# Optimization experiments

Measured on AMD Instinct MI355X. Metric: run time of the kernel, lower is better.

## Reference

```python
import jax, jax.numpy as jnp
import numpy as np

A = 32          # num input capsule types
PSIZE = 16      # caps_size (pose matrix 4x4)
MD = 4          # mat_dim = sqrt(caps_size)
NCLS = 10       # output capsules / classes
KF = 5          # routing kernel (final_shape)
KK = KF * KF
KKA = KK * A
ITERS = 3
FINAL_LAMBDA = 0.01
EPS = 1e-12
LN2PI = float(np.log(2.0 * np.pi))
BN_EPS = 1e-5


def unfold(x, k, stride, pad):
    # torch.nn.functional.unfold: [b,C,h,w] -> [b, C*k*k, L], (c, kh, kw) channel-major
    b, c, h, w = x.shape
    if pad:
        x = jnp.pad(x, ((0, 0), (0, 0), (pad, pad), (pad, pad)))
    oh = (h + 2 * pad - k) // stride + 1
    ow = (w + 2 * pad - k) // stride + 1
    cols = jnp.stack([
        jnp.stack([x[:, :, i:i + stride * oh:stride, j:j + stride * ow:stride]
                   for j in range(k)], axis=3)
        for i in range(k)], axis=2)          # [b, c, k, k, oh, ow]
    return cols.reshape(b, c * k * k, oh * ow)


def conv3x3(x, w):
    return jax.lax.conv_general_dilated(x, w, (1, 1), [(1, 1), (1, 1)],
                                        dimension_numbers=('NCHW', 'OIHW', 'NCHW'))


def bn_inf(x, g, b, m, v):
    scale = g / jnp.sqrt(v + BN_EPS)
    return (x - m[None, :, None, None]) * scale[None, :, None, None] + b[None, :, None, None]


def em_routing(a_in, pose, W, beta_u, beta_a):
    b = a_in.shape[0]
    # pose votes
    pu = unfold(pose, KF, 1, 0)                     # [b, A*PSIZE*KK, l]
    l = pu.shape[-1]
    pu = pu.reshape(b, A, PSIZE, KK, l).transpose(0, 4, 3, 1, 2).reshape(b, l, KKA, PSIZE)
    pm = pu.reshape(b, l, KKA, MD, MD)[:, :, :, None]        # [b,l,kkA,1,md,md]
    v = jnp.matmul(pm, W)                                    # [b,l,kkA,B,md,md]
    v = v.reshape(b, l, KKA, NCLS, PSIZE)
    # activations
    au = unfold(a_in, KF, 1, 0).reshape(b, A, KK, l).transpose(0, 3, 2, 1).reshape(b, l, KKA)
    r = jnp.ones((b, l, KKA, NCLS, 1), v.dtype)
    a_out = mu = None
    for i in range(ITERS):
        lam = FINAL_LAMBDA * (1.0 - 0.95 ** (i + 1))
        # M-step
        rw = r * au[:, :, :, None, None]
        r_sum = rw.sum(axis=2, keepdims=True)                # [b,l,1,B,1]
        coeff = rw / (r_sum + EPS)
        mu = (coeff * v).sum(axis=2, keepdims=True)          # [b,l,1,B,psize]
        sigma_sq = (coeff * (v - mu) ** 2).sum(axis=2, keepdims=True) + EPS
        r_s = r_sum[:, :, 0]                                 # [b,l,B,1]
        sig = sigma_sq[:, :, 0]                              # [b,l,B,psize]
        cost_h = (beta_u + 0.5 * jnp.log(sig)) * r_s         # log(sqrt(s)) = 0.5*log(s)
        a_out = jax.nn.sigmoid(lam * (beta_a - cost_h.sum(axis=3)))   # [b,l,B]
        if i < ITERS - 1:
            # E-step (note: log(sigma_sq * ln2pi) as in original code)
            ln_p = (-0.5 * jnp.sum(jnp.log(sigma_sq * LN2PI), axis=-1)
                    - jnp.sum((v - mu) ** 2 / (2.0 * sigma_sq), axis=-1))   # [b,l,kkA,B]
            ln_ap = ln_p + jnp.log(a_out)[:, :, None, :]
            r = jax.nn.softmax(ln_ap, axis=-1)[..., None]
    oh = int(np.floor(np.sqrt(l)))
    pose_out = mu[:, :, 0].reshape(b, l, -1).transpose(0, 2, 1).reshape(b, -1, oh, oh)
    a_map = a_out.transpose(0, 2, 1).reshape(b, -1, oh, oh)
    return a_map, pose_out


def setup_inputs():
    key = jax.random.key(0)
    ks = jax.random.split(key, 14)
    batch = 256
    x = jax.random.normal(ks[0], (batch, 512, 5, 5), jnp.float32)
    w_a = jax.random.normal(ks[1], (A, 512, 3, 3), jnp.float32) * 0.02
    w_pose = jax.random.normal(ks[2], (A * PSIZE, 512, 3, 3), jnp.float32) * 0.02
    bn_a_g = 1.0 + 0.1 * jax.random.normal(ks[3], (A,), jnp.float32)
    bn_a_b = 0.1 * jax.random.normal(ks[4], (A,), jnp.float32)
    bn_a_m = 0.1 * jax.random.normal(ks[5], (A,), jnp.float32)
    bn_a_v = jax.random.uniform(ks[6], (A,), jnp.float32, 0.5, 1.5)
    C2 = A * PSIZE
    bn_p_g = 1.0 + 0.1 * jax.random.normal(ks[7], (C2,), jnp.float32)
    bn_p_b = 0.1 * jax.random.normal(ks[8], (C2,), jnp.float32)
    bn_p_m = 0.1 * jax.random.normal(ks[9], (C2,), jnp.float32)
    bn_p_v = jax.random.uniform(ks[10], (C2,), jnp.float32, 0.5, 1.5)
    W = jax.random.normal(ks[11], (KKA, NCLS, MD, MD), jnp.float32) * 0.25
    beta_u = jnp.zeros((1, 1, NCLS, 1), jnp.float32)
    beta_a = jnp.zeros((1, 1, NCLS), jnp.float32)
    return {"x": x, "w_a": w_a, "w_pose": w_pose,
            "bn_a_g": bn_a_g, "bn_a_b": bn_a_b, "bn_a_m": bn_a_m, "bn_a_v": bn_a_v,
            "bn_p_g": bn_p_g, "bn_p_b": bn_p_b, "bn_p_m": bn_p_m, "bn_p_v": bn_p_v,
            "W": W, "beta_u": beta_u, "beta_a": beta_a}


def reference(x, w_a, w_pose, bn_a_g, bn_a_b, bn_a_m, bn_a_v,
              bn_p_g, bn_p_b, bn_p_m, bn_p_v, W, beta_u, beta_a):
    a = jax.nn.sigmoid(bn_inf(conv3x3(x, w_a), bn_a_g, bn_a_b, bn_a_m, bn_a_v))
    pose = bn_inf(conv3x3(x, w_pose), bn_p_g, bn_p_b, bn_p_m, bn_p_v)
    a_map, _ = em_routing(a, pose, W, beta_u, beta_a)
    out = a_map.reshape(a_map.shape[0], -1)          # [b, 10]
    out = out / out.sum(axis=1, keepdims=True)
    return jnp.log(out)
```

## Files before the change

kernel.cpp:

```cpp
#include <hip/hip_runtime.h>
#include <math.h>

#define CIN 512
#define NCLS 10
#define KDIM 4608
#define NTOT 6400
#define MPAD 640
#define BK 128
#define NKT 36
#define NABLK (5 * NKT)
#define LN2PI_F 1.8378770664093453f

typedef __attribute__((ext_vector_type(8))) short bf16x8;
typedef __attribute__((ext_vector_type(4))) float f32x4;

typedef const __attribute__((address_space(1))) void* gas_ptr;
typedef __attribute__((address_space(3))) void* las_ptr;

__device__ __forceinline__ void async_copy16(const void* g, void* l) {
    __builtin_amdgcn_global_load_lds((gas_ptr)g, (las_ptr)l, 16, 0, 0);
}

__device__ __forceinline__ unsigned short f2bf(float f) {
    unsigned int u = __float_as_uint(f);
    u = (u + 0x7fffu + ((u >> 16) & 1u)) >> 16;
    return (unsigned short)u;
}
__device__ __forceinline__ float fexp(float x) { return __expf(x); }
__device__ __forceinline__ float flog(float x) { return __logf(x); }

__global__ __launch_bounds__(256) void pack_a_kernel(
    const float* __restrict__ w_pose, const float* __restrict__ w_a,
    const float* __restrict__ bn_p_g, const float* __restrict__ bn_p_b,
    const float* __restrict__ bn_p_m, const float* __restrict__ bn_p_v,
    const float* __restrict__ bn_a_g, const float* __restrict__ bn_a_b,
    const float* __restrict__ bn_a_m, const float* __restrict__ bn_a_v,
    const float* __restrict__ Wm,
    unsigned short* __restrict__ At, unsigned short* __restrict__ Wmb,
    float* __restrict__ sc, float* __restrict__ bi)
{
    const int blk = blockIdx.x;
    const int t = threadIdx.x;

    if (blk >= NABLK) {
        const int chunk = (blk - NABLK) * 256 + t;
        if (chunk < 16000) {
            const float4* s4 = reinterpret_cast<const float4*>(Wm + (size_t)chunk * 8);
            float4 x0 = s4[0], x1 = s4[1];
            int4 o;
            o.x = (int)f2bf(x0.x) | ((int)f2bf(x0.y) << 16);
            o.y = (int)f2bf(x0.z) | ((int)f2bf(x0.w) << 16);
            o.z = (int)f2bf(x1.x) | ((int)f2bf(x1.y) << 16);
            o.w = (int)f2bf(x1.z) | ((int)f2bf(x1.w) << 16);
            reinterpret_cast<int4*>(Wmb + (size_t)chunk * 8)[0] = o;
        }
        return;
    }

    const int mblk = blk / NKT;
    if (blk == 0) {
        for (int i = t; i < MPAD; i += 256) {
            float s = 0.f, b = 0.f;
            if (i < 512) {
                s = bn_p_g[i] / sqrtf(bn_p_v[i] + 1e-5f);
                b = bn_p_b[i] - bn_p_m[i] * s;
            } else if (i < 544) {
                const int j = i - 512;
                s = bn_a_g[j] / sqrtf(bn_a_v[j] + 1e-5f);
                b = bn_a_b[j] - bn_a_m[j] * s;
            }
            sc[i] = s; bi[i] = b;
        }
    }

    const int kt = blk - mblk * NKT;
    #pragma unroll
    for (int j = 0; j < 8; ++j) {
        const int c = t + j * 256;
        const int kc8 = c >> 7, slot = c & 127;
        const int row = mblk * 128 + (slot ^ (kc8 << 2));
        const int k0 = (kt * 16 + kc8) * 8;
        float v[8] = {0.f,0.f,0.f,0.f,0.f,0.f,0.f,0.f};
        if (row < 512) {
            const float4* s4 = reinterpret_cast<const float4*>(w_pose + (size_t)row * KDIM + k0);
            float4 x0 = s4[0], x1 = s4[1];
            v[0]=x0.x; v[1]=x0.y; v[2]=x0.z; v[3]=x0.w;
            v[4]=x1.x; v[5]=x1.y; v[6]=x1.z; v[7]=x1.w;
        } else if (row < 544) {
            const float4* s4 = reinterpret_cast<const float4*>(w_a + (size_t)(row - 512) * KDIM + k0);
            float4 x0 = s4[0], x1 = s4[1];
            v[0]=x0.x; v[1]=x0.y; v[2]=x0.z; v[3]=x0.w;
            v[4]=x1.x; v[5]=x1.y; v[6]=x1.z; v[7]=x1.w;
        }
        int4 o;
        o.x = (int)f2bf(v[0]) | ((int)f2bf(v[1]) << 16);
        o.y = (int)f2bf(v[2]) | ((int)f2bf(v[3]) << 16);
        o.z = (int)f2bf(v[4]) | ((int)f2bf(v[5]) << 16);
        o.w = (int)f2bf(v[6]) | ((int)f2bf(v[7]) << 16);
        reinterpret_cast<int4*>(At + ((((size_t)blk) << 11) + c) * 8)[0] = o;
    }
}

__global__ __launch_bounds__(1024) void pack_b_kernel(
    const float* __restrict__ x, unsigned short* __restrict__ Bt)
{
    __shared__ __align__(16) float xs[CIN * 25];
    const int b = blockIdx.x;
    const int t = threadIdx.x;
    const float4* xb = reinterpret_cast<const float4*>(x + (size_t)b * (CIN * 25));
    for (int f4 = t; f4 < (CIN * 25) / 4; f4 += 1024)
        reinterpret_cast<float4*>(xs)[f4] = xb[f4];
    __syncthreads();

    for (int w = t; w < 25 * (KDIM / 8); w += 1024) {
        const int px = w / (KDIM / 8);
        const int ch = w - px * (KDIM / 8);
        const int py = px / 5, qx = px % 5;
        const int k0 = ch * 8;
        unsigned short v[8];
        #pragma unroll
        for (int j = 0; j < 8; ++j) {
            const int k = k0 + j;
            const int ci = k / 9;
            const int kk = k - ci * 9;
            const int dy = kk / 3, dx = kk - dy * 3;
            const int yy = py + dy - 1, xx = qx + dx - 1;
            const bool ok = (yy >= 0) & (yy < 5) & (xx >= 0) & (xx < 5);
            v[j] = ok ? f2bf(xs[ci * 25 + yy * 5 + xx]) : (unsigned short)0;
        }
        int4 o;
        o.x = (int)v[0] | ((int)v[1] << 16);
        o.y = (int)v[2] | ((int)v[3] << 16);
        o.z = (int)v[4] | ((int)v[5] << 16);
        o.w = (int)v[6] | ((int)v[7] << 16);
        const int n = b * 25 + px;
        const int nblk = n >> 7, nr = n & 127;
        const int kt = k0 >> 7;
        const int kc8 = (k0 >> 3) & 15;
        const int c = kc8 * 128 + (nr ^ (kc8 << 2));
        reinterpret_cast<int4*>(Bt + ((((size_t)(nblk * NKT + kt)) << 11) + c) * 8)[0] = o;
    }
}

__global__ __launch_bounds__(512) void gemm_kernel(
    const unsigned short* __restrict__ At,
    const unsigned short* __restrict__ Bt,
    const float* __restrict__ sc, const float* __restrict__ bi,
    float* __restrict__ C)
{
    __shared__ __align__(16) unsigned char smem[131072];
    const int t = threadIdx.x;
    const int mblk = blockIdx.x, nblk = blockIdx.y;
    const int m0 = mblk * 128, n0 = nblk * 128;
    const int lane = t & 63, w = t >> 6;
    const int g = w >> 2, wq = w & 3;
    const int wm = wq >> 1, wn = wq & 1;
    const int row16 = lane & 15, quad = lane >> 4;

    f32x4 acc[4][4] = {};

    const unsigned short* gAbase = At + (((size_t)mblk * NKT) << 14);
    const unsigned short* gBbase = Bt + (((size_t)nblk * NKT) << 14);

    #define STAGE(kt, s)                                                      \
    {                                                                         \
        unsigned short* As_ = (unsigned short*)(smem + (s) * 65536);          \
        unsigned short* Bs_ = As_ + 16384;                                    \
        const unsigned short* ga = gAbase + ((size_t)(kt) << 14);             \
        const unsigned short* gb = gBbase + ((size_t)(kt) << 14);             \
        _Pragma("unroll")                                                     \
        for (int j = 0; j < 4; ++j) {                                         \
            async_copy16(ga + ((size_t)(j * 512 + t) << 3),                   \
                         As_ + ((size_t)(j * 512 + w * 64) << 3));            \
            async_copy16(gb + ((size_t)(j * 512 + t) << 3),                   \
                         Bs_ + ((size_t)(j * 512 + w * 64) << 3));            \
        }                                                                     \
    }

    #define COMPUTE(s)                                                        \
    {                                                                         \
        const unsigned short* As_ = (const unsigned short*)(smem + (s) * 65536);\
        const unsigned short* Bs_ = As_ + 16384;                              \
        _Pragma("unroll")                                                     \
        for (int ks = 0; ks < 2; ++ks) {                                      \
            const int kc8b = g * 8 + ks * 4 + quad;                           \
            const int sw = kc8b << 2;                                         \
            bf16x8 af[4], bfr[4];                                             \
            _Pragma("unroll")                                                 \
            for (int mt = 0; mt < 4; ++mt)                                    \
                af[mt] = *reinterpret_cast<const bf16x8*>(                    \
                    &As_[(size_t)(kc8b * 128 + ((wm * 64 + mt * 16 + row16) ^ sw)) * 8]);\
            _Pragma("unroll")                                                 \
            for (int nt = 0; nt < 4; ++nt)                                    \
                bfr[nt] = *reinterpret_cast<const bf16x8*>(                   \
                    &Bs_[(size_t)(kc8b * 128 + ((wn * 64 + nt * 16 + row16) ^ sw)) * 8]);\
            _Pragma("unroll")                                                 \
            for (int mt = 0; mt < 4; ++mt)                                    \
                _Pragma("unroll")                                             \
                for (int nt = 0; nt < 4; ++nt)                                \
                    acc[mt][nt] = __builtin_amdgcn_mfma_f32_16x16x32_bf16(    \
                        af[mt], bfr[nt], acc[mt][nt], 0, 0, 0);               \
        }                                                                     \
    }

    STAGE(0, 0);
    for (int kt = 0; kt < NKT; ++kt) {
        __syncthreads();
        if (kt + 1 < NKT) STAGE(kt + 1, (kt + 1) & 1);
        COMPUTE(kt & 1);
    }
    #undef STAGE
    #undef COMPUTE

    float* mb = (float*)smem;
    #pragma unroll
    for (int rnd = 0; rnd < 2; ++rnd) {
        __syncthreads();
        if (g == 1 && (wq >> 1) == rnd) {
            f32x4* dst = (f32x4*)(mb + (wq & 1) * 4096);
            #pragma unroll
            for (int i = 0; i < 16; ++i)
                dst[i * 64 + lane] = acc[i >> 2][i & 3];
        }
        __syncthreads();
        if (g == 0 && (wq >> 1) == rnd) {
            const f32x4* src = (const f32x4*)(mb + (wq & 1) * 4096);
            #pragma unroll
            for (int i = 0; i < 16; ++i)
                acc[i >> 2][i & 3] += src[i * 64 + lane];
        }
    }

    if (g == 0) {
        #pragma unroll
        for (int mt = 0; mt < 4; ++mt) {
            const int mbase = m0 + wm * 64 + mt * 16 + quad * 4;
            if (mbase >= 544) continue;
            #pragma unroll
            for (int rg = 0; rg < 4; ++rg) {
                const int m = mbase + rg;
                const float s = sc[m], bbx = bi[m];
                const bool is_a = (m >= 512);
                #pragma unroll
                for (int nt = 0; nt < 4; ++nt) {
                    const int n = n0 + wn * 64 + nt * 16 + row16;
                    float v = fmaf(acc[mt][nt][rg], s, bbx);
                    if (is_a) v = 1.f / (1.f + fexp(-v));
                    C[(size_t)m * NTOT + n] = v;
                }
            }
        }
    }
}

__device__ __forceinline__ void loadW_bf(const unsigned short* wp, float* wv) {
    const int4* q = reinterpret_cast<const int4*>(wp);
    const int4 q0 = q[0], q1 = q[1];
    const unsigned int u[8] = {(unsigned)q0.x,(unsigned)q0.y,(unsigned)q0.z,(unsigned)q0.w,
                               (unsigned)q1.x,(unsigned)q1.y,(unsigned)q1.z,(unsigned)q1.w};
    #pragma unroll
    for (int i = 0; i < 8; ++i) {
        wv[2*i]   = __uint_as_float(u[i] << 16);
        wv[2*i+1] = __uint_as_float(u[i] & 0xFFFF0000u);
    }
}

__global__ __launch_bounds__(640, 1) void em_kernel(
    const float* __restrict__ C,
    const unsigned short* __restrict__ Wmb,
    const float* __restrict__ beta_u, const float* __restrict__ beta_a,
    float* __restrict__ out)
{
    __shared__ __align__(16) float psh[25][32][20];
    __shared__ float aush[800];
    __shared__ float lnqp[2][NCLS][800];
    __shared__ float mu_sh[NCLS][16];
    __shared__ float i2s_sh[NCLS][16];
    __shared__ float costp[2][NCLS];
    __shared__ float slgp[2][NCLS];
    __shared__ float Kc_sh[NCLS];
    __shared__ float aout_sh[NCLS];

    const int b = blockIdx.x, t = threadIdx.x;
    const int rh = (t >= 320) ? 1 : 0;
    const int th = t - rh * 320;
    const int c = th >> 5, a = th & 31;
    float* rwsh = &lnqp[1][0][0];

    const float* pb = C + (size_t)b * 25;
    for (int f = t; f < 12800; f += 640) {
        const int c2 = f / 25, px = f - c2 * 25;
        psh[px][c2 >> 4][c2 & 15] = pb[(size_t)c2 * NTOT + px];
    }
    const float* ab = C + (size_t)512 * NTOT + (size_t)b * 25;
    for (int f = t; f < 800; f += 640) {
        const int ci = f / 25, px = f - ci * 25;
        aush[px * 32 + ci] = ab[(size_t)ci * NTOT + px];
    }
    __syncthreads();

    const float bu = beta_u[c], ba = beta_a[c];
    float muL[8], i2sL[8], KcL = 0.f;
    const unsigned short* wbase = Wmb + ((size_t)a * NCLS + c) * 16;

    #define VOTE_HALF(kk, vv)                                                \
        float pm[8], wv[16];                                                 \
        {                                                                    \
            const float4* pr = reinterpret_cast<const float4*>(&psh[kk][a][rh * 8]); \
            const float4 p0 = pr[0], p1 = pr[1];                             \
            pm[0]=p0.x; pm[1]=p0.y; pm[2]=p0.z; pm[3]=p0.w;                  \
            pm[4]=p1.x; pm[5]=p1.y; pm[6]=p1.z; pm[7]=p1.w;                  \
            loadW_bf(wbase + (size_t)(kk) * 5120, wv);                       \
            _Pragma("unroll")                                                \
            for (int jr = 0; jr < 2; ++jr) {                                 \
                _Pragma("unroll")                                            \
                for (int s = 0; s < 4; ++s) {                                \
                    float av = 0.f;                                          \
                    _Pragma("unroll")                                        \
                    for (int tt = 0; tt < 4; ++tt)                           \
                        av = fmaf(pm[jr*4+tt], wv[tt*4+s], av);              \
                    vv[jr*4+s] = av;                                         \
                }                                                            \
            }                                                                \
        }

    float p95 = 1.f;
    for (int it = 0; it < 3; ++it) {
        p95 *= 0.95f;
        const float lam = 0.01f * (1.f - p95);

        if (it > 0) {
            for (int kk = 0; kk < 25; ++kk) {
                float vv[8];
                VOTE_HALF(kk, vv);
                float q = (rh == 0) ? KcL : 0.f;
                #pragma unroll
                for (int j = 0; j < 8; ++j) {
                    const float d = vv[j] - muL[j];
                    q -= d * d * i2sL[j];
                }
                lnqp[rh][c][kk * 32 + a] = q;
            }
            __syncthreads();
            {
                float* l0 = &lnqp[0][0][0];
                const float* l1 = &lnqp[1][0][0];
                for (int f = t; f < 8000; f += 640) l0[f] += l1[f];
            }
            __syncthreads();
            {
                const int k0 = rh ? 13 : 0, k1 = rh ? 25 : 13;
                for (int kk = k0; kk < k1; ++kk) {
                    const int m = kk * 32 + a;
                    float qv[NCLS];
                    #pragma unroll
                    for (int cc = 0; cc < NCLS; ++cc) qv[cc] = lnqp[0][cc][m];
                    float mx = qv[0];
                    #pragma unroll
                    for (int cc = 1; cc < NCLS; ++cc) mx = fmaxf(mx, qv[cc]);
                    float den = 0.f;
                    #pragma unroll
                    for (int cc = 0; cc < NCLS; ++cc) den += fexp(qv[cc] - mx);
                    rwsh[c * 800 + m] = fexp(qv[c] - mx) * __builtin_amdgcn_rcpf(den)
                                        * aush[m];
                }
            }
            __syncthreads();
        }

        float S0 = 0.f, S1[8], S2[8];
        #pragma unroll
        for (int j = 0; j < 8; ++j) { S1[j] = 0.f; S2[j] = 0.f; }

        for (int kk = 0; kk < 25; ++kk) {
            float vv[8];
            VOTE_HALF(kk, vv);
            const int m = kk * 32 + a;
            const float rw = (it == 0) ? aush[m] : rwsh[c * 800 + m];
            S0 += rw;
            #pragma unroll
            for (int j = 0; j < 8; ++j) {
                const float rv = rw * vv[j];
                S1[j] += rv;
                S2[j] = fmaf(rv, vv[j], S2[j]);
            }
        }

        #pragma unroll
        for (int off = 16; off >= 1; off >>= 1) {
            S0 += __shfl_xor(S0, off);
            #pragma unroll
            for (int j = 0; j < 8; ++j) {
                S1[j] += __shfl_xor(S1[j], off);
                S2[j] += __shfl_xor(S2[j], off);
            }
        }

        if (a == 0) {
            const float s0e = S0 + 1e-12f;
            const float inv = 1.f / s0e;
            float cost_ = 0.f, slg_ = 0.f;
            #pragma unroll
            for (int j = 0; j < 8; ++j) {
                const float mu_ = S1[j] * inv;
                const float sg = (S2[j] - 2.f * mu_ * S1[j] + mu_ * mu_ * S0) * inv
                                 + 1e-12f;
                cost_ += bu + 0.5f * flog(sg);
                slg_ += flog(sg * LN2PI_F);
                mu_sh[c][rh * 8 + j] = mu_;
                i2s_sh[c][rh * 8 + j] = 0.5f / sg;
            }
            costp[rh][c] = cost_;
            slgp[rh][c] = slg_;
        }
        __syncthreads();
        if (a == 0 && rh == 0) {
            const float costsum = (costp[0][c] + costp[1][c]) * S0;
            const float aout = 1.f / (1.f + fexp(-(lam * (ba - costsum))));
            aout_sh[c] = aout;
            Kc_sh[c] = flog(aout) - 0.5f * (slgp[0][c] + slgp[1][c]);
        }
        __syncthreads();
        if (it < 2) {
            #pragma unroll
            for (int j = 0; j < 8; ++j) {
                muL[j] = mu_sh[c][rh * 8 + j];
                i2sL[j] = i2s_sh[c][rh * 8 + j];
            }
            KcL = Kc_sh[c];
        }
    }

    if (t < NCLS) {
        float s = 0.f;
        #pragma unroll
        for (int cc = 0; cc < NCLS; ++cc) s += aout_sh[cc];
        out[b * NCLS + t] = flog(aout_sh[t] / s);
    }
    #undef VOTE_HALF
}

extern "C" void kernel_launch(void* const* d_in, const int* in_sizes, int n_in,
                              void* d_out, int out_size, void* d_ws, size_t ws_size,
                              hipStream_t stream) {
    const float* x      = (const float*)d_in[0];
    const float* w_a    = (const float*)d_in[1];
    const float* w_pose = (const float*)d_in[2];
    const float* bn_a_g = (const float*)d_in[3];
    const float* bn_a_b = (const float*)d_in[4];
    const float* bn_a_m = (const float*)d_in[5];
    const float* bn_a_v = (const float*)d_in[6];
    const float* bn_p_g = (const float*)d_in[7];
    const float* bn_p_b = (const float*)d_in[8];
    const float* bn_p_m = (const float*)d_in[9];
    const float* bn_p_v = (const float*)d_in[10];
    const float* Wm     = (const float*)d_in[11];
    const float* beta_u = (const float*)d_in[12];
    const float* beta_a = (const float*)d_in[13];
    float* out = (float*)d_out;

    char* p = (char*)d_ws;
    unsigned short* At  = (unsigned short*)p;  p += (size_t)MPAD * KDIM * 2;
    unsigned short* Bt  = (unsigned short*)p;  p += (size_t)NTOT * KDIM * 2;
    unsigned short* Wmb = (unsigned short*)p;  p += (size_t)800 * NCLS * 16 * 2;
    float* C  = (float*)p;                     p += (size_t)544 * NTOT * 4;
    float* sc = (float*)p;                     p += MPAD * 4;
    float* bi = (float*)p;                     p += MPAD * 4;

    pack_a_kernel<<<NABLK + 63, 256, 0, stream>>>(w_pose, w_a,
                                                  bn_p_g, bn_p_b, bn_p_m, bn_p_v,
                                                  bn_a_g, bn_a_b, bn_a_m, bn_a_v,
                                                  Wm, At, Wmb, sc, bi);
    pack_b_kernel<<<256, 1024, 0, stream>>>(x, Bt);
    dim3 gg(MPAD / 128, NTOT / 128);
    gemm_kernel<<<gg, 512, 0, stream>>>(At, Bt, sc, bi, C);
    em_kernel<<<256, 640, 0, stream>>>(C, Wmb, beta_u, beta_a, out);
}
```

Baseline: 264.6 us.

## Split E-step by kernel position instead of pose halves, prefetch W and pose loads

The E-step log-likelihood is now computed per kernel-position half, with each thread covering all 16 pose elements, instead of per pose-element half. This drops the second lnq buffer and the extra reduction pass with its barrier, and halves shared-memory use for that stage. Responsibilities are kept in registers and written back in place after a barrier. Both loops now software-prefetch the next W and pose values from global and shared memory. The cost is more registers per thread (16-element votes plus a 13-entry rst array) with 640 threads in a block.

```diff
diff --git a/kernel.cpp b/kernel.cpp
--- a/kernel.cpp
+++ b/kernel.cpp
@@ -253,11 +253,9 @@
     }
 }
 
-__device__ __forceinline__ void loadW_bf(const unsigned short* wp, float* wv) {
-    const int4* q = reinterpret_cast<const int4*>(wp);
-    const int4 q0 = q[0], q1 = q[1];
-    const unsigned int u[8] = {(unsigned)q0.x,(unsigned)q0.y,(unsigned)q0.z,(unsigned)q0.w,
-                               (unsigned)q1.x,(unsigned)q1.y,(unsigned)q1.z,(unsigned)q1.w};
+__device__ __forceinline__ void unpack16(const int4& w0, const int4& w1, float* wv) {
+    const unsigned int u[8] = {(unsigned)w0.x,(unsigned)w0.y,(unsigned)w0.z,(unsigned)w0.w,
+                               (unsigned)w1.x,(unsigned)w1.y,(unsigned)w1.z,(unsigned)w1.w};
     #pragma unroll
     for (int i = 0; i < 8; ++i) {
         wv[2*i]   = __uint_as_float(u[i] << 16);
@@ -273,19 +271,19 @@
 {
     __shared__ __align__(16) float psh[25][32][20];
     __shared__ float aush[800];
-    __shared__ float lnqp[2][NCLS][800];
-    __shared__ float mu_sh[NCLS][16];
-    __shared__ float i2s_sh[NCLS][16];
+    __shared__ float lnq[NCLS][800];
+    __shared__ float2 muis[NCLS][16];
     __shared__ float costp[2][NCLS];
     __shared__ float slgp[2][NCLS];
     __shared__ float Kc_sh[NCLS];
     __shared__ float aout_sh[NCLS];
 
     const int b = blockIdx.x, t = threadIdx.x;
-    const int rh = (t >= 320) ? 1 : 0;
-    const int th = t - rh * 320;
+    const int h = (t >= 320) ? 1 : 0;
+    const int th = t - h * 320;
     const int c = th >> 5, a = th & 31;
-    float* rwsh = &lnqp[1][0][0];
+    const int k0 = h ? 13 : 0;
+    const int nk = h ? 12 : 13;
 
     const float* pb = C + (size_t)b * 25;
     for (int f = t; f < 12800; f += 640) {
@@ -300,29 +298,7 @@
     __syncthreads();
 
     const float bu = beta_u[c], ba = beta_a[c];
-    float muL[8], i2sL[8], KcL = 0.f;
     const unsigned short* wbase = Wmb + ((size_t)a * NCLS + c) * 16;
-
-    #define VOTE_HALF(kk, vv)                                                \
-        float pm[8], wv[16];                                                 \
-        {                                                                    \
-            const float4* pr = reinterpret_cast<const float4*>(&psh[kk][a][rh * 8]); \
-            const float4 p0 = pr[0], p1 = pr[1];                             \
-            pm[0]=p0.x; pm[1]=p0.y; pm[2]=p0.z; pm[3]=p0.w;                  \
-            pm[4]=p1.x; pm[5]=p1.y; pm[6]=p1.z; pm[7]=p1.w;                  \
-            loadW_bf(wbase + (size_t)(kk) * 5120, wv);                       \
-            _Pragma("unroll")                                                \
-            for (int jr = 0; jr < 2; ++jr) {                                 \
-                _Pragma("unroll")                                            \
-                for (int s = 0; s < 4; ++s) {                                \
-                    float av = 0.f;                                          \
-                    _Pragma("unroll")                                        \
-                    for (int tt = 0; tt < 4; ++tt)                           \
-                        av = fmaf(pm[jr*4+tt], wv[tt*4+s], av);              \
-                    vv[jr*4+s] = av;                                         \
-                }                                                            \
-            }                                                                \
-        }
 
     float p95 = 1.f;
     for (int it = 0; it < 3; ++it) {
@@ -330,59 +306,105 @@
         const float lam = 0.01f * (1.f - p95);
 
         if (it > 0) {
-            for (int kk = 0; kk < 25; ++kk) {
-                float vv[8];
-                VOTE_HALF(kk, vv);
-                float q = (rh == 0) ? KcL : 0.f;
+            const float KcL = Kc_sh[c];
+            const unsigned short* wp = wbase + (size_t)k0 * 5120;
+            int4 wr0 = *reinterpret_cast<const int4*>(wp);
+            int4 wr1 = *reinterpret_cast<const int4*>(wp + 8);
+            for (int i = 0; i < nk; ++i) {
+                const int kk = k0 + i;
+                const int4 w0 = wr0, w1 = wr1;
+                if (i + 1 < nk) {
+                    const unsigned short* wn = wbase + (size_t)(kk + 1) * 5120;
+                    wr0 = *reinterpret_cast<const int4*>(wn);
+                    wr1 = *reinterpret_cast<const int4*>(wn + 8);
+                }
+                const float4 q0 = *reinterpret_cast<const float4*>(&psh[kk][a][0]);
+                const float4 q1 = *reinterpret_cast<const float4*>(&psh[kk][a][4]);
+                const float4 q2 = *reinterpret_cast<const float4*>(&psh[kk][a][8]);
+                const float4 q3 = *reinterpret_cast<const float4*>(&psh[kk][a][12]);
+                const float pm[16] = {q0.x,q0.y,q0.z,q0.w, q1.x,q1.y,q1.z,q1.w,
+                                      q2.x,q2.y,q2.z,q2.w, q3.x,q3.y,q3.z,q3.w};
+                float wv[16];
+                unpack16(w0, w1, wv);
+                float q = KcL;
                 #pragma unroll
-                for (int j = 0; j < 8; ++j) {
-                    const float d = vv[j] - muL[j];
-                    q -= d * d * i2sL[j];
+                for (int r = 0; r < 4; ++r) {
+                    #pragma unroll
+                    for (int s = 0; s < 4; ++s) {
+                        float v = 0.f;
+                        #pragma unroll
+                        for (int t4 = 0; t4 < 4; ++t4)
+                            v = fmaf(pm[r*4+t4], wv[t4*4+s], v);
+                        const float2 mi = muis[c][r*4+s];
+                        const float d = v - mi.x;
+                        q = fmaf(-d * d, mi.y, q);
+                    }
                 }
-                lnqp[rh][c][kk * 32 + a] = q;
+                lnq[c][kk * 32 + a] = q;
             }
             __syncthreads();
-            {
-                float* l0 = &lnqp[0][0][0];
-                const float* l1 = &lnqp[1][0][0];
-                for (int f = t; f < 8000; f += 640) l0[f] += l1[f];
-            }
-            __syncthreads();
-            {
-                const int k0 = rh ? 13 : 0, k1 = rh ? 25 : 13;
-                for (int kk = k0; kk < k1; ++kk) {
-                    const int m = kk * 32 + a;
+
+            float rst[13];
+            #pragma unroll
+            for (int i = 0; i < 13; ++i) {
+                if (i < nk) {
+                    const int m = (k0 + i) * 32 + a;
                     float qv[NCLS];
                     #pragma unroll
-                    for (int cc = 0; cc < NCLS; ++cc) qv[cc] = lnqp[0][cc][m];
+                    for (int cc = 0; cc < NCLS; ++cc) qv[cc] = lnq[cc][m];
                     float mx = qv[0];
                     #pragma unroll
                     for (int cc = 1; cc < NCLS; ++cc) mx = fmaxf(mx, qv[cc]);
                     float den = 0.f;
                     #pragma unroll
                     for (int cc = 0; cc < NCLS; ++cc) den += fexp(qv[cc] - mx);
-                    rwsh[c * 800 + m] = fexp(qv[c] - mx) * __builtin_amdgcn_rcpf(den)
-                                        * aush[m];
+                    rst[i] = fexp(qv[c] - mx) * __builtin_amdgcn_rcpf(den) * aush[m];
                 }
             }
             __syncthreads();
-        }
-
+            #pragma unroll
+            for (int i = 0; i < 13; ++i)
+                if (i < nk) lnq[c][(k0 + i) * 32 + a] = rst[i];
+            __syncthreads();
+        }
+
+        const float* rwp = (it == 0) ? aush : &lnq[c][0];
         float S0 = 0.f, S1[8], S2[8];
         #pragma unroll
         for (int j = 0; j < 8; ++j) { S1[j] = 0.f; S2[j] = 0.f; }
 
+        int4 wr0 = *reinterpret_cast<const int4*>(wbase);
+        int4 wr1 = *reinterpret_cast<const int4*>(wbase + 8);
+        float4 pr0 = *reinterpret_cast<const float4*>(&psh[0][a][h * 8]);
+        float4 pr1 = *reinterpret_cast<const float4*>(&psh[0][a][h * 8 + 4]);
         for (int kk = 0; kk < 25; ++kk) {
-            float vv[8];
-            VOTE_HALF(kk, vv);
-            const int m = kk * 32 + a;
-            const float rw = (it == 0) ? aush[m] : rwsh[c * 800 + m];
+            const int4 w0 = wr0, w1 = wr1;
+            const float4 p0 = pr0, p1 = pr1;
+            const float rw = rwp[kk * 32 + a];
+            if (kk < 24) {
+                const unsigned short* wn = wbase + (size_t)(kk + 1) * 5120;
+                wr0 = *reinterpret_cast<const int4*>(wn);
+                wr1 = *reinterpret_cast<const int4*>(wn + 8);
+                pr0 = *reinterpret_cast<const float4*>(&psh[kk + 1][a][h * 8]);
+                pr1 = *reinterpret_cast<const float4*>(&psh[kk + 1][a][h * 8 + 4]);
+            }
+            float wv[16];
+            unpack16(w0, w1, wv);
+            const float pm8[8] = {p0.x,p0.y,p0.z,p0.w, p1.x,p1.y,p1.z,p1.w};
             S0 += rw;
             #pragma unroll
-            for (int j = 0; j < 8; ++j) {
-                const float rv = rw * vv[j];
-                S1[j] += rv;
-                S2[j] = fmaf(rv, vv[j], S2[j]);
+            for (int jr = 0; jr < 2; ++jr) {
+                #pragma unroll
+                for (int s = 0; s < 4; ++s) {
+                    float v = 0.f;
+                    #pragma unroll
+                    for (int t4 = 0; t4 < 4; ++t4)
+                        v = fmaf(pm8[jr*4+t4], wv[t4*4+s], v);
+                    const int j = jr * 4 + s;
+                    const float rv = rw * v;
+                    S1[j] += rv;
+                    S2[j] = fmaf(rv, v, S2[j]);
+                }
             }
         }
 
@@ -407,28 +429,19 @@
                                  + 1e-12f;
                 cost_ += bu + 0.5f * flog(sg);
                 slg_ += flog(sg * LN2PI_F);
-                mu_sh[c][rh * 8 + j] = mu_;
-                i2s_sh[c][rh * 8 + j] = 0.5f / sg;
-            }
-            costp[rh][c] = cost_;
-            slgp[rh][c] = slg_;
+                muis[c][h * 8 + j] = make_float2(mu_, 0.5f / sg);
+            }
+            costp[h][c] = cost_;
+            slgp[h][c] = slg_;
         }
         __syncthreads();
-        if (a == 0 && rh == 0) {
+        if (a == 0 && h == 0) {
             const float costsum = (costp[0][c] + costp[1][c]) * S0;
             const float aout = 1.f / (1.f + fexp(-(lam * (ba - costsum))));
             aout_sh[c] = aout;
             Kc_sh[c] = flog(aout) - 0.5f * (slgp[0][c] + slgp[1][c]);
         }
         __syncthreads();
-        if (it < 2) {
-            #pragma unroll
-            for (int j = 0; j < 8; ++j) {
-                muL[j] = mu_sh[c][rh * 8 + j];
-                i2sL[j] = i2s_sh[c][rh * 8 + j];
-            }
-            KcL = Kc_sh[c];
-        }
     }
 
     if (t < NCLS) {
@@ -437,7 +450,6 @@
         for (int cc = 0; cc < NCLS; ++cc) s += aout_sh[cc];
         out[b * NCLS + t] = flog(aout_sh[t] / s);
     }
-    #undef VOTE_HALF
 }
 
 extern "C" void kernel_launch(void* const* d_in, const int* in_sizes, int n_in,
```

After: 272.1 us. +2.8%, slower.

## Store pose GEMM output in bf16 and remap GEMM block order

Applied to the files above, without the earlier changes.

The GEMM now writes the 512 pose channels as bf16 into a separate buffer and the 32 activation channels as fp32 into another. The EM kernel reads the bf16 poses and converts them back to float. This halves the bytes of the pose intermediate passed between kernels. The GEMM grid also becomes a linear 250-block launch with a custom mapping that groups blocks by n-tile chunks, likely for cache locality. The cost is lower precision on the pose values feeding routing.

```diff
diff --git a/kernel.cpp b/kernel.cpp
--- a/kernel.cpp
+++ b/kernel.cpp
@@ -25,6 +25,9 @@
     unsigned int u = __float_as_uint(f);
     u = (u + 0x7fffu + ((u >> 16) & 1u)) >> 16;
     return (unsigned short)u;
+}
+__device__ __forceinline__ float bf2f(unsigned short s) {
+    return __uint_as_float(((unsigned int)s) << 16);
 }
 __device__ __forceinline__ float fexp(float x) { return __expf(x); }
 __device__ __forceinline__ float flog(float x) { return __logf(x); }
@@ -146,11 +149,16 @@
     const unsigned short* __restrict__ At,
     const unsigned short* __restrict__ Bt,
     const float* __restrict__ sc, const float* __restrict__ bi,
-    float* __restrict__ C)
+    unsigned short* __restrict__ Cp,
+    float* __restrict__ Ca)
 {
     __shared__ __align__(16) unsigned char smem[131072];
     const int t = threadIdx.x;
-    const int mblk = blockIdx.x, nblk = blockIdx.y;
+    const int L = blockIdx.x;
+    int mblk, nblk;
+    if (L >= 240) { const int i = L - 240; mblk = i >> 1; nblk = 48 + (i & 1); }
+    else          { const int q = L / 40, r = L - q * 40;
+                    mblk = r >> 3; nblk = q * 8 + (r & 7); }
     const int m0 = mblk * 128, n0 = nblk * 128;
     const int lane = t & 63, w = t >> 6;
     const int g = w >> 2, wq = w & 3;
@@ -240,13 +248,12 @@
             for (int rg = 0; rg < 4; ++rg) {
                 const int m = mbase + rg;
                 const float s = sc[m], bbx = bi[m];
-                const bool is_a = (m >= 512);
                 #pragma unroll
                 for (int nt = 0; nt < 4; ++nt) {
                     const int n = n0 + wn * 64 + nt * 16 + row16;
-                    float v = fmaf(acc[mt][nt][rg], s, bbx);
-                    if (is_a) v = 1.f / (1.f + fexp(-v));
-                    C[(size_t)m * NTOT + n] = v;
+                    const float v = fmaf(acc[mt][nt][rg], s, bbx);
+                    if (m < 512) Cp[(size_t)m * NTOT + n] = f2bf(v);
+                    else Ca[(size_t)(m - 512) * NTOT + n] = 1.f / (1.f + fexp(-v));
                 }
             }
         }
@@ -266,7 +273,8 @@
 }
 
 __global__ __launch_bounds__(640, 1) void em_kernel(
-    const float* __restrict__ C,
+    const unsigned short* __restrict__ Cp,
+    const float* __restrict__ Ca,
     const unsigned short* __restrict__ Wmb,
     const float* __restrict__ beta_u, const float* __restrict__ beta_a,
     float* __restrict__ out)
@@ -287,12 +295,12 @@
     const int c = th >> 5, a = th & 31;
     float* rwsh = &lnqp[1][0][0];
 
-    const float* pb = C + (size_t)b * 25;
+    const unsigned short* pb = Cp + (size_t)b * 25;
     for (int f = t; f < 12800; f += 640) {
         const int c2 = f / 25, px = f - c2 * 25;
-        psh[px][c2 >> 4][c2 & 15] = pb[(size_t)c2 * NTOT + px];
-    }
-    const float* ab = C + (size_t)512 * NTOT + (size_t)b * 25;
+        psh[px][c2 >> 4][c2 & 15] = bf2f(pb[(size_t)c2 * NTOT + px]);
+    }
+    const float* ab = Ca + (size_t)b * 25;
     for (int f = t; f < 800; f += 640) {
         const int ci = f / 25, px = f - ci * 25;
         aush[px * 32 + ci] = ab[(size_t)ci * NTOT + px];
@@ -463,7 +471,8 @@
     unsigned short* At  = (unsigned short*)p;  p += (size_t)MPAD * KDIM * 2;
     unsigned short* Bt  = (unsigned short*)p;  p += (size_t)NTOT * KDIM * 2;
     unsigned short* Wmb = (unsigned short*)p;  p += (size_t)800 * NCLS * 16 * 2;
-    float* C  = (float*)p;                     p += (size_t)544 * NTOT * 4;
+    unsigned short* Cp  = (unsigned short*)p;  p += (size_t)512 * NTOT * 2;
+    float* Ca = (float*)p;                     p += (size_t)32 * NTOT * 4;
     float* sc = (float*)p;                     p += MPAD * 4;
     float* bi = (float*)p;                     p += MPAD * 4;
 
@@ -472,7 +481,6 @@
                                                   bn_a_g, bn_a_b, bn_a_m, bn_a_v,
                                                   Wm, At, Wmb, sc, bi);
     pack_b_kernel<<<256, 1024, 0, stream>>>(x, Bt);
-    dim3 gg(MPAD / 128, NTOT / 128);
-    gemm_kernel<<<gg, 512, 0, stream>>>(At, Bt, sc, bi, C);
-    em_kernel<<<256, 640, 0, stream>>>(C, Wmb, beta_u, beta_a, out);
-}
+    gemm_kernel<<<250, 512, 0, stream>>>(At, Bt, sc, bi, Cp, Ca);
+    em_kernel<<<256, 640, 0, stream>>>(Cp, Ca, Wmb, beta_u, beta_a, out);
+}
```

Result: faster. 258.0 us (-2.5%).
